# Performance work log

Measured on AMD Instinct MI355X. Metric: run time of the kernel, lower is better.

Reference implementation:

```python
import jax, jax.numpy as jnp
import numpy as np

LAMBDA_SOFTMAX = 9.0
LAMBDA_LSE = 6.0
EPS = 1e-8
LEAKY_SLOPE = 0.1


def setup_inputs() -> dict:
    key = jax.random.key(0)
    k1, k2, k3, k4 = jax.random.split(key, 4)
    B, R, L, D = 256, 36, 40, 1024  # n_image=n_caption=B, n_regions, max_words, embed
    return {
        'pool_img': jax.random.normal(k1, (B, D), jnp.float32),
        'img_emb': jax.random.normal(k2, (B, R, D), jnp.float32),
        'pool_txt': jax.random.normal(k3, (B, D), jnp.float32),
        'cap_emb': jax.random.normal(k4, (B, L, D), jnp.float32),
    }


def _l2norm(x, axis):
    return x / (jnp.sqrt(jnp.sum(x * x, axis=axis, keepdims=True)) + EPS)


def _lse_reduce(m):
    # mul_(lambda_lse).exp_() ; sum over singleton dim ; log / lambda_lse
    return jnp.log(jnp.exp(m * LAMBDA_LSE)) / LAMBDA_LSE


def _text_score_one(cap_i, txt_poo_i, images):
    # cap_i: (L, d) query; images: (B, R, d) context. clipped_l2norm variant.
    attn = jnp.einsum('brd,ld->brl', images, cap_i)            # (B, R, L)
    attn = jax.nn.leaky_relu(attn, LEAKY_SLOPE)
    attn = _l2norm(attn, axis=2)                               # l2norm over queryL
    attn = jnp.swapaxes(attn, 1, 2)                            # (B, L, R)
    attn = jax.nn.softmax(attn * LAMBDA_SOFTMAX, axis=-1)      # softmax over regions
    wctx = jnp.einsum('blr,brd->bld', attn, images)            # (B, L, d)
    w12 = jnp.einsum('bld,d->bl', wctx, txt_poo_i)
    w1 = jnp.sqrt(jnp.sum(txt_poo_i * txt_poo_i))
    w2 = jnp.sqrt(jnp.sum(wctx * wctx, axis=2))
    sim = w12 / jnp.maximum(w1 * w2, EPS)                      # (B, L)
    return _lse_reduce(jnp.mean(sim, axis=1))                  # (B,)


def _image_score_one(cap_i, img_emb, img_poo):
    # query: img_emb (B, R, d); context: cap_i (L, d) broadcast over B.
    attn = jnp.einsum('ld,brd->blr', cap_i, img_emb)           # (B, L, R)
    attn = jax.nn.leaky_relu(attn, LEAKY_SLOPE)
    attn = _l2norm(attn, axis=2)                               # l2norm over regions
    attn = jnp.swapaxes(attn, 1, 2)                            # (B, R, L)
    attn = jax.nn.softmax(attn * LAMBDA_SOFTMAX, axis=-1)      # softmax over words
    wctx = jnp.einsum('brl,ld->brd', attn, cap_i)              # (B, R, d)
    w12 = jnp.einsum('brd,bd->br', wctx, img_poo)
    w1 = jnp.sqrt(jnp.sum(img_poo * img_poo, axis=1, keepdims=True))  # (B,1)
    w2 = jnp.sqrt(jnp.sum(wctx * wctx, axis=2))                # (B, R)
    sim = w12 / jnp.maximum(w1 * w2, EPS)
    return _lse_reduce(jnp.mean(sim, axis=1))                  # (B,)


def reference(pool_img, img_emb, pool_txt, cap_emb):
    # scores_t2i: loop over captions -> vmap; result (n_cap, n_image) -> transpose
    t2i = jax.vmap(_text_score_one, in_axes=(0, 0, None))(cap_emb, pool_txt, img_emb).T
    i2t = jax.vmap(_image_score_one, in_axes=(0, None, None))(cap_emb, img_emb, pool_img).T
    base = pool_img @ pool_txt.T
    return t2i + i2t + base
```

## Files before the change

kernel.cpp:

```cpp
#include <hip/hip_runtime.h>

typedef unsigned short u16;
typedef __attribute__((ext_vector_type(8))) short bf16x8;
typedef __attribute__((ext_vector_type(4))) float f32x4;

#define D_EMB 1024
#define NBAT  256
#define AS1 __attribute__((address_space(1)))
#define AS3 __attribute__((address_space(3)))

__device__ __forceinline__ u16 f2bf(float f){
    unsigned int u = __float_as_uint(f);
    unsigned int r = (u + 0x7fffu + ((u >> 16) & 1u)) >> 16;
    return (u16)r;
}
__device__ __forceinline__ float leaky(float x){ return x > 0.f ? x : 0.1f * x; }

__device__ __forceinline__ unsigned pack2(float a, float b){
    return (__float_as_uint(a) >> 16) | (__float_as_uint(b) & 0xffff0000u);
}
__device__ __forceinline__ float unpk_lo(unsigned p){ return __uint_as_float(p << 16); }
__device__ __forceinline__ float unpk_hi(unsigned p){ return __uint_as_float(p & 0xffff0000u); }

__global__ void pack_kernel(const float* __restrict__ pool_img, const float* __restrict__ img_emb,
                            const float* __restrict__ pool_txt, const float* __restrict__ cap_emb,
                            u16* __restrict__ imgw, u16* __restrict__ capw){
    int row = blockIdx.x;
    const float* src; u16* dst;
    if (row < NBAT * 37){
        int e = row / 37, rr = row - e * 37;
        src = (rr < 36) ? (img_emb + ((size_t)e * 36 + rr) * D_EMB) : (pool_img + (size_t)e * D_EMB);
        dst = imgw + (size_t)row * D_EMB;
    } else {
        int r2 = row - NBAT * 37;
        int e = r2 / 41, rr = r2 - e * 41;
        src = (rr < 40) ? (cap_emb + ((size_t)e * 40 + rr) * D_EMB) : (pool_txt + (size_t)e * D_EMB);
        dst = capw + (size_t)r2 * D_EMB;
    }
    int t = threadIdx.x;
    float4 v = ((const float4*)src)[t];
    unsigned long long pk = (unsigned long long)f2bf(v.x)
        | ((unsigned long long)f2bf(v.y) << 16)
        | ((unsigned long long)f2bf(v.z) << 32)
        | ((unsigned long long)f2bf(v.w) << 48);
    *(unsigned long long*)(dst + (size_t)t * 4) = pk;
}

__global__ void norm_kernel(const float* __restrict__ pool_img, const float* __restrict__ pool_txt,
                            float* __restrict__ w1i, float* __restrict__ w1t){
    __shared__ float red[256];
    int v = blockIdx.x;
    const float* src = (v < 256) ? (pool_img + (size_t)v * D_EMB)
                                 : (pool_txt + (size_t)(v - 256) * D_EMB);
    int t = threadIdx.x;
    float4 x = ((const float4*)src)[t];
    red[t] = x.x*x.x + x.y*x.y + x.z*x.z + x.w*x.w;
    __syncthreads();
    for (int off = 128; off > 0; off >>= 1){
        if (t < off) red[t] += red[t + off];
        __syncthreads();
    }
    if (t == 0){
        float n = sqrtf(red[0]);
        if (v < 256) w1i[v] = n; else w1t[v - 256] = n;
    }
}

__launch_bounds__(256, 2)
__global__ void gram_kernel(const u16* __restrict__ imgw, const u16* __restrict__ capw,
                            float* __restrict__ G, float* __restrict__ H){
    __shared__ __align__(16) char gsm[6144];
    int blk = blockIdx.x;
    int tid = threadIdx.x, lane = tid & 63;
    int wave = __builtin_amdgcn_readfirstlane(tid >> 6);
    int frow = lane & 15, q = lane >> 4;

    const u16* E; float* Gout; int R;
    if (blk < NBAT){ E = imgw + (size_t)blk * 37 * D_EMB; Gout = G + (size_t)blk * 1296; R = 36; }
    else { int b = blk - NBAT; E = capw + (size_t)b * 41 * D_EMB; Gout = H + (size_t)b * 1600; R = 40; }

    {
        uint4 z = {0u,0u,0u,0u};
        for (int off = tid * 16; off < 6144; off += 4096) *(uint4*)(gsm + off) = z;
    }

    const u16* gsrc[2]; int goff[2]; bool gval[2];
    #pragma unroll
    for (int j = 0; j < 2; ++j){
        int g = wave + j * 4;
        gval[j] = false; gsrc[j] = E; goff[j] = 0;
        if (g < 6){
            int kk = g / 3, t = g - kk * 3;
            int row = t * 16 + frow;
            gsrc[j] = E + (size_t)row * D_EMB + kk * 32 + q * 8;
            goff[j] = g * 1024;
            gval[j] = (row < R);
        }
    }

    int wm = wave >> 1, wn = wave & 1;
    int nTm = wm ? 1 : 2, nTn = wn ? 1 : 2;
    f32x4 acc[2][2];
    #pragma unroll
    for (int a = 0; a < 2; ++a)
        #pragma unroll
        for (int b = 0; b < 2; ++b) acc[a][b] = (f32x4){0.f,0.f,0.f,0.f};

    for (int c = 0; c < 16; ++c){
        __syncthreads();
        #pragma unroll
        for (int j = 0; j < 2; ++j){
            if (gval[j]){
                __builtin_amdgcn_global_load_lds(
                    (const AS1 void*)(const void*)(gsrc[j] + c * 64),
                    (AS3 void*)(void*)(gsm + goff[j] + lane * 16),
                    16, 0, 0);
            }
        }
        __syncthreads();
        #pragma unroll
        for (int kk = 0; kk < 2; ++kk){
            bf16x8 fA[2], fB[2];
            #pragma unroll
            for (int mi = 0; mi < 2; ++mi)
                if (mi < nTm) fA[mi] = *(const bf16x8*)(gsm + ((kk * 3 + (wm + mi * 2)) * 64 + lane) * 16);
            #pragma unroll
            for (int ni = 0; ni < 2; ++ni)
                if (ni < nTn) fB[ni] = *(const bf16x8*)(gsm + ((kk * 3 + (wn + ni * 2)) * 64 + lane) * 16);
            #pragma unroll
            for (int mi = 0; mi < 2; ++mi)
                if (mi < nTm)
                    #pragma unroll
                    for (int ni = 0; ni < 2; ++ni)
                        if (ni < nTn)
                            acc[mi][ni] = __builtin_amdgcn_mfma_f32_16x16x32_bf16(
                                fA[mi], fB[ni], acc[mi][ni], 0, 0, 0);
        }
    }

    #pragma unroll
    for (int mi = 0; mi < 2; ++mi){
        if (mi < nTm){
            int tm = wm + mi * 2;
            #pragma unroll
            for (int ni = 0; ni < 2; ++ni){
                if (ni < nTn){
                    int tn = wn + ni * 2;
                    int col = tn * 16 + frow;
                    if (col < R){
                        #pragma unroll
                        for (int g = 0; g < 4; ++g){
                            int row = tm * 16 + q * 4 + g;
                            if (row < R) Gout[row * R + col] = acc[mi][ni][g];
                        }
                    }
                }
            }
        }
    }
}

__launch_bounds__(256, 5)
__global__ void fused_kernel(const u16* __restrict__ imgw, const u16* __restrict__ capw,
                             const float* __restrict__ G, const float* __restrict__ H,
                             const float* __restrict__ w1i, const float* __restrict__ w1t,
                             float* __restrict__ out){
    __shared__ __align__(16) char smem[26624];
    float* Call = (float*)smem;
    float* rnb  = (float*)(smem + 25160);
    float* cnb  = (float*)(smem + 25736);

    int tid  = threadIdx.x;
    int lane = tid & 63;
    int wave = __builtin_amdgcn_readfirstlane(tid >> 6);
    int frow = lane & 15, q = lane >> 4;

    int lin = blockIdx.x;
    int xcd = lin & 7;
    int s   = lin >> 3;
    int b_t = (xcd << 4) | (s & 15);
    int i_t = s >> 4;
    int b0 = b_t * 2, i0 = i_t * 2;
    const u16* Ag = imgw + (size_t)b0 * 37 * D_EMB;
    const u16* Bg = capw + (size_t)i0 * 41 * D_EMB;

    {
        uint4 z = {0u,0u,0u,0u};
        for (int off = tid * 16; off < 22528; off += 4096) *(uint4*)(smem + off) = z;
    }

    const u16* gsrc[6]; int goff[6]; bool gval[6];
    #pragma unroll
    for (int j = 0; j < 6; ++j){
        int g = wave + j * 4;
        gval[j] = false; gsrc[j] = Ag; goff[j] = 0;
        if (g < 22){
            if (g < 10){
                int tm = g % 5, kk = g / 5;
                int row = tm * 16 + frow;
                gsrc[j] = Ag + (size_t)row * D_EMB + kk * 32 + q * 8;
                goff[j] = g * 1024;
                gval[j] = (row < 74);
            } else {
                int gb = g - 10;
                int tn = gb % 6, kk = gb / 6;
                int row = tn * 16 + frow;
                gsrc[j] = Bg + (size_t)row * D_EMB + kk * 32 + q * 8;
                goff[j] = 10240 + gb * 1024;
                gval[j] = (row < 82);
            }
        }
    }

    int wm = wave >> 1, wn = wave & 1;
    int nTm = wm ? 2 : 3;
    f32x4 acc[3][3];
    #pragma unroll
    for (int aa = 0; aa < 3; ++aa)
        #pragma unroll
        for (int bb = 0; bb < 3; ++bb) acc[aa][bb] = (f32x4){0.f, 0.f, 0.f, 0.f};

    for (int c = 0; c < 16; ++c){
        __syncthreads();
        #pragma unroll
        for (int j = 0; j < 6; ++j){
            if (gval[j]){
                __builtin_amdgcn_global_load_lds(
                    (const AS1 void*)(const void*)(gsrc[j] + c * 64),
                    (AS3 void*)(void*)(smem + goff[j] + lane * 16),
                    16, 0, 0);
            }
        }
        __syncthreads();
        #pragma unroll
        for (int kk = 0; kk < 2; ++kk){
            bf16x8 bfr[3];
            #pragma unroll
            for (int ni = 0; ni < 3; ++ni){
                int tn = wn + ni * 2;
                bfr[ni] = *(const bf16x8*)(smem + 10240 + ((kk * 6 + tn) * 64 + lane) * 16);
            }
            #pragma unroll
            for (int mi = 0; mi < 3; ++mi){
                if (mi < nTm){
                    int tm = wm + mi * 2;
                    bf16x8 af = *(const bf16x8*)(smem + ((kk * 5 + tm) * 64 + lane) * 16);
                    #pragma unroll
                    for (int ni = 0; ni < 3; ++ni){
                        acc[mi][ni] = __builtin_amdgcn_mfma_f32_16x16x32_bf16(
                            af, bfr[ni], acc[mi][ni], 0, 0, 0);
                    }
                }
            }
        }
    }
    __syncthreads();

    #pragma unroll
    for (int mi = 0; mi < 3; ++mi){
        if (mi < nTm){
            int tm = wm + mi * 2;
            #pragma unroll
            for (int ni = 0; ni < 3; ++ni){
                int tn = wn + ni * 2;
                int col = tn * 16 + frow;
                int rbase = tm * 16 + q * 4;
                if (col < 82){
                    #pragma unroll
                    for (int g = 0; g < 4; ++g){
                        int rowc = rbase + g;
                        if (rowc < 74) Call[rowc * 85 + col] = acc[mi][ni][g];
                    }
                }
            }
        }
    }
    __syncthreads();

    int pb = wave >> 1, pi = wave & 1;
    int bg = b0 + pb, ig = i0 + pi;
    const float* Sv = Call + (pb * 37) * 85 + pi * 41;
    const float* Gb = G + (size_t)bg * 1296;
    const float* Hi = H + (size_t)ig * 1600;

    {
        int r0 = (lane < 36) ? lane : 35;
        float s2 = 0.f;
        #pragma unroll
        for (int l = 0; l < 40; ++l){ float x = leaky(Sv[r0 * 85 + l]); s2 = fmaf(x, x, s2); }
        if (lane < 36) rnb[wave * 36 + lane] = 1.f / (sqrtf(s2) + 1e-8f);
    }
    float t2i_sum;
    {
        int lc = (lane < 40) ? lane : 39;
        unsigned up[18];
        float dd = 0.f, num = 0.f;
        #pragma unroll
        for (int r = 0; r < 36; r += 2){
            float x0 = leaky(Sv[r * 85 + lc]);
            float e0 = __expf(9.0f * x0 * rnb[wave * 36 + r]);
            float x1 = leaky(Sv[(r + 1) * 85 + lc]);
            float e1 = __expf(9.0f * x1 * rnb[wave * 36 + r + 1]);
            dd += e0 + e1;
            num = fmaf(e0, Sv[r * 85 + 40], fmaf(e1, Sv[(r + 1) * 85 + 40], num));
            up[r >> 1] = pack2(e0, e1);
        }
        float zz = 0.f;
        #pragma unroll
        for (int rr = 0; rr < 36; ++rr){
            float urr = (rr & 1) ? unpk_hi(up[rr >> 1]) : unpk_lo(up[rr >> 1]);
            float t = 0.f;
            #pragma unroll
            for (int r2 = rr + 1; r2 < 36; ++r2){
                float ur2 = (r2 & 1) ? unpk_hi(up[r2 >> 1]) : unpk_lo(up[r2 >> 1]);
                t = fmaf(Gb[rr * 36 + r2], ur2, t);
            }
            zz += (2.f * t + Gb[rr * 36 + rr] * urr) * urr;
        }
        float w2s = sqrtf(fmaxf(zz, 0.f));
        float sim = num / fmaxf(w1t[ig] * w2s, 1e-8f);
        sim = (lane < 40) ? sim : 0.f;
        #pragma unroll
        for (int off = 32; off > 0; off >>= 1) sim += __shfl_down(sim, off);
        t2i_sum = sim;
    }

    {
        int l0 = (lane < 40) ? lane : 39;
        float s2 = 0.f;
        #pragma unroll
        for (int r = 0; r < 36; ++r){ float x = leaky(Sv[r * 85 + l0]); s2 = fmaf(x, x, s2); }
        if (lane < 40) cnb[wave * 40 + lane] = 1.f / (sqrtf(s2) + 1e-8f);
    }
    float i2t_sum;
    {
        int rc = (lane < 36) ? lane : 35;
        unsigned vp[20];
        float dd = 0.f, num = 0.f;
        #pragma unroll
        for (int l = 0; l < 40; l += 2){
            float x0 = leaky(Sv[rc * 85 + l]);
            float e0 = __expf(9.0f * x0 * cnb[wave * 40 + l]);
            float x1 = leaky(Sv[rc * 85 + l + 1]);
            float e1 = __expf(9.0f * x1 * cnb[wave * 40 + l + 1]);
            dd += e0 + e1;
            num = fmaf(e0, Sv[36 * 85 + l], fmaf(e1, Sv[36 * 85 + l + 1], num));
            vp[l >> 1] = pack2(e0, e1);
        }
        float zz = 0.f;
        #pragma unroll
        for (int ll = 0; ll < 40; ++ll){
            float vll = (ll & 1) ? unpk_hi(vp[ll >> 1]) : unpk_lo(vp[ll >> 1]);
            float t = 0.f;
            #pragma unroll
            for (int l2 = ll + 1; l2 < 40; ++l2){
                float vl2 = (l2 & 1) ? unpk_hi(vp[l2 >> 1]) : unpk_lo(vp[l2 >> 1]);
                t = fmaf(Hi[ll * 40 + l2], vl2, t);
            }
            zz += (2.f * t + Hi[ll * 40 + ll] * vll) * vll;
        }
        float w2s = sqrtf(fmaxf(zz, 0.f));
        float sim = num / fmaxf(w1i[bg] * w2s, 1e-8f);
        sim = (lane < 36) ? sim : 0.f;
        #pragma unroll
        for (int off = 32; off > 0; off >>= 1) sim += __shfl_down(sim, off);
        i2t_sum = sim;
    }

    if (lane == 0)
        out[bg * 256 + ig] = t2i_sum * (1.f / 40.f) + i2t_sum * (1.f / 36.f) + Sv[36 * 85 + 40];
}

extern "C" void kernel_launch(void* const* d_in, const int* in_sizes, int n_in,
                              void* d_out, int out_size, void* d_ws, size_t ws_size,
                              hipStream_t stream){
    const float* pool_img = (const float*)d_in[0];
    const float* img_emb  = (const float*)d_in[1];
    const float* pool_txt = (const float*)d_in[2];
    const float* cap_emb  = (const float*)d_in[3];
    float* out = (float*)d_out;

    char* ws = (char*)d_ws;
    size_t o = 0;
    u16* imgw = (u16*)(ws + o);  o += (size_t)256 * 37 * 1024 * 2;
    u16* capw = (u16*)(ws + o);  o += (size_t)256 * 41 * 1024 * 2;
    float* G  = (float*)(ws + o); o += (size_t)256 * 36 * 36 * 4;
    float* H  = (float*)(ws + o); o += (size_t)256 * 40 * 40 * 4;
    float* w1i = (float*)(ws + o); o += 1024;
    float* w1t = (float*)(ws + o); o += 1024;

    pack_kernel<<<19968, 256, 0, stream>>>(pool_img, img_emb, pool_txt, cap_emb, imgw, capw);
    norm_kernel<<<512, 256, 0, stream>>>(pool_img, pool_txt, w1i, w1t);
    gram_kernel<<<512, 256, 0, stream>>>(imgw, capw, G, H);
    fused_kernel<<<16384, 256, 0, stream>>>(imgw, capw, G, H, w1i, w1t, out);
}
```

Before: 750.6 us.

## Replace per-pair Gram quadratic forms with Cholesky factors and MFMA norms

Adds a kernel that Cholesky-factorizes each per-image and per-caption Gram matrix and stores the factors in bf16. The fused kernel then computes each weighted-context norm as ||u^T L||^2 using bf16 MFMA instructions on attention weights staged in swizzled shared memory, replacing the scalar triangular quadratic-form loops. The aim is to move the dominant O(R^2) per-lane FMA work onto matrix cores. It adds a small extra launch, lowers the occupancy hint from 5 to 4, and adds bf16 rounding of the factors and of the exp weights in the MFMA path.

```diff
diff --git a/kernel.cpp b/kernel.cpp
--- a/kernel.cpp
+++ b/kernel.cpp
@@ -19,8 +19,6 @@
 __device__ __forceinline__ unsigned pack2(float a, float b){
     return (__float_as_uint(a) >> 16) | (__float_as_uint(b) & 0xffff0000u);
 }
-__device__ __forceinline__ float unpk_lo(unsigned p){ return __uint_as_float(p << 16); }
-__device__ __forceinline__ float unpk_hi(unsigned p){ return __uint_as_float(p & 0xffff0000u); }
 
 __global__ void pack_kernel(const float* __restrict__ pool_img, const float* __restrict__ img_emb,
                             const float* __restrict__ pool_txt, const float* __restrict__ cap_emb,
@@ -160,9 +158,44 @@
     }
 }
 
-__launch_bounds__(256, 5)
+template<int R>
+__device__ __forceinline__ void chol_wave(const float* __restrict__ src,
+                                          u16* __restrict__ dst, int lane){
+    int r = lane;
+    bool act = (r < R);
+    const float* row = src + (size_t)(act ? r : 0) * R;
+    float a[R];
+    #pragma unroll
+    for (int k = 0; k < R; ++k) a[k] = act ? row[k] : 0.f;
+    #pragma unroll
+    for (int j = 0; j < R; ++j){
+        float ajj = __shfl(a[j], j);
+        float inv = (ajj > 1e-12f) ? rsqrtf(ajj) : 0.f;
+        float lrj = a[j] * inv;
+        if (r < j || !act) lrj = 0.f;
+        dst[j * 64 + lane] = f2bf(lrj);
+        #pragma unroll
+        for (int k = j + 1; k < R; ++k){
+            float lkj = __shfl(lrj, k);
+            a[k] = fmaf(-lrj, lkj, a[k]);
+        }
+    }
+    #pragma unroll
+    for (int j = R; j < 48; ++j) dst[j * 64 + lane] = 0;
+}
+
+__global__ void chol_kernel(const float* __restrict__ G, const float* __restrict__ H,
+                            u16* __restrict__ Lbi, u16* __restrict__ Lbc){
+    int lane = threadIdx.x & 63;
+    int wave = threadIdx.x >> 6;
+    int id = blockIdx.x * 4 + wave;
+    if (id < NBAT) chol_wave<36>(G + (size_t)id * 1296, Lbi + (size_t)id * 3072, lane);
+    else           chol_wave<40>(H + (size_t)(id - NBAT) * 1600, Lbc + (size_t)(id - NBAT) * 3072, lane);
+}
+
+__launch_bounds__(256, 4)
 __global__ void fused_kernel(const u16* __restrict__ imgw, const u16* __restrict__ capw,
-                             const float* __restrict__ G, const float* __restrict__ H,
+                             const u16* __restrict__ Lbi, const u16* __restrict__ Lbc,
                              const float* __restrict__ w1i, const float* __restrict__ w1t,
                              float* __restrict__ out){
     __shared__ __align__(16) char smem[26624];
@@ -280,8 +313,8 @@
     int pb = wave >> 1, pi = wave & 1;
     int bg = b0 + pb, ig = i0 + pi;
     const float* Sv = Call + (pb * 37) * 85 + pi * 41;
-    const float* Gb = G + (size_t)bg * 1296;
-    const float* Hi = H + (size_t)ig * 1600;
+    const u16* Lb_t2i = Lbi + (size_t)bg * 3072;
+    const u16* Lb_i2t = Lbc + (size_t)ig * 3072;
 
     {
         int r0 = (lane < 36) ? lane : 35;
@@ -290,41 +323,6 @@
         for (int l = 0; l < 40; ++l){ float x = leaky(Sv[r0 * 85 + l]); s2 = fmaf(x, x, s2); }
         if (lane < 36) rnb[wave * 36 + lane] = 1.f / (sqrtf(s2) + 1e-8f);
     }
-    float t2i_sum;
-    {
-        int lc = (lane < 40) ? lane : 39;
-        unsigned up[18];
-        float dd = 0.f, num = 0.f;
-        #pragma unroll
-        for (int r = 0; r < 36; r += 2){
-            float x0 = leaky(Sv[r * 85 + lc]);
-            float e0 = __expf(9.0f * x0 * rnb[wave * 36 + r]);
-            float x1 = leaky(Sv[(r + 1) * 85 + lc]);
-            float e1 = __expf(9.0f * x1 * rnb[wave * 36 + r + 1]);
-            dd += e0 + e1;
-            num = fmaf(e0, Sv[r * 85 + 40], fmaf(e1, Sv[(r + 1) * 85 + 40], num));
-            up[r >> 1] = pack2(e0, e1);
-        }
-        float zz = 0.f;
-        #pragma unroll
-        for (int rr = 0; rr < 36; ++rr){
-            float urr = (rr & 1) ? unpk_hi(up[rr >> 1]) : unpk_lo(up[rr >> 1]);
-            float t = 0.f;
-            #pragma unroll
-            for (int r2 = rr + 1; r2 < 36; ++r2){
-                float ur2 = (r2 & 1) ? unpk_hi(up[r2 >> 1]) : unpk_lo(up[r2 >> 1]);
-                t = fmaf(Gb[rr * 36 + r2], ur2, t);
-            }
-            zz += (2.f * t + Gb[rr * 36 + rr] * urr) * urr;
-        }
-        float w2s = sqrtf(fmaxf(zz, 0.f));
-        float sim = num / fmaxf(w1t[ig] * w2s, 1e-8f);
-        sim = (lane < 40) ? sim : 0.f;
-        #pragma unroll
-        for (int off = 32; off > 0; off >>= 1) sim += __shfl_down(sim, off);
-        t2i_sum = sim;
-    }
-
     {
         int l0 = (lane < 40) ? lane : 39;
         float s2 = 0.f;
@@ -332,43 +330,161 @@
         for (int r = 0; r < 36; ++r){ float x = leaky(Sv[r * 85 + l0]); s2 = fmaf(x, x, s2); }
         if (lane < 40) cnb[wave * 40 + lane] = 1.f / (sqrtf(s2) + 1e-8f);
     }
-    float i2t_sum;
+
+    unsigned up[18]; float num1 = 0.f;
+    {
+        int lc = (lane < 40) ? lane : 39;
+        #pragma unroll
+        for (int r = 0; r < 36; r += 2){
+            float x0 = leaky(Sv[r * 85 + lc]) * rnb[wave * 36 + r];
+            float x1 = leaky(Sv[(r + 1) * 85 + lc]) * rnb[wave * 36 + r + 1];
+            float e0 = __expf(9.0f * x0), e1 = __expf(9.0f * x1);
+            num1 = fmaf(e0, Sv[r * 85 + 40], fmaf(e1, Sv[(r + 1) * 85 + 40], num1));
+            up[r >> 1] = pack2(e0, e1);
+        }
+    }
+    unsigned vp[20]; float num2 = 0.f;
     {
         int rc = (lane < 36) ? lane : 35;
-        unsigned vp[20];
-        float dd = 0.f, num = 0.f;
         #pragma unroll
         for (int l = 0; l < 40; l += 2){
-            float x0 = leaky(Sv[rc * 85 + l]);
-            float e0 = __expf(9.0f * x0 * cnb[wave * 40 + l]);
-            float x1 = leaky(Sv[rc * 85 + l + 1]);
-            float e1 = __expf(9.0f * x1 * cnb[wave * 40 + l + 1]);
-            dd += e0 + e1;
-            num = fmaf(e0, Sv[36 * 85 + l], fmaf(e1, Sv[36 * 85 + l + 1], num));
+            float x0 = leaky(Sv[rc * 85 + l]) * cnb[wave * 40 + l];
+            float x1 = leaky(Sv[rc * 85 + l + 1]) * cnb[wave * 40 + l + 1];
+            float e0 = __expf(9.0f * x0), e1 = __expf(9.0f * x1);
+            num2 = fmaf(e0, Sv[36 * 85 + l], fmaf(e1, Sv[36 * 85 + l + 1], num2));
             vp[l >> 1] = pack2(e0, e1);
         }
-        float zz = 0.f;
-        #pragma unroll
-        for (int ll = 0; ll < 40; ++ll){
-            float vll = (ll & 1) ? unpk_hi(vp[ll >> 1]) : unpk_lo(vp[ll >> 1]);
-            float t = 0.f;
-            #pragma unroll
-            for (int l2 = ll + 1; l2 < 40; ++l2){
-                float vl2 = (l2 & 1) ? unpk_hi(vp[l2 >> 1]) : unpk_lo(vp[l2 >> 1]);
-                t = fmaf(Hi[ll * 40 + l2], vl2, t);
-            }
-            zz += (2.f * t + Hi[ll * 40 + ll] * vll) * vll;
-        }
-        float w2s = sqrtf(fmaxf(zz, 0.f));
-        float sim = num / fmaxf(w1i[bg] * w2s, 1e-8f);
-        sim = (lane < 36) ? sim : 0.f;
-        #pragma unroll
-        for (int off = 32; off > 0; off >>= 1) sim += __shfl_down(sim, off);
-        i2t_sum = sim;
+    }
+    float base = Sv[36 * 85 + 40];
+    __syncthreads();
+
+    char* slice = smem + wave * 6144;
+    int sxw = lane & 7;
+
+    if (lane < 40){
+        char* rp = slice + lane * 128;
+        #pragma unroll
+        for (int jj = 0; jj < 9; ++jj){
+            int slot = jj >> 1, wi = (jj & 1) * 8;
+            uint2 w; w.x = up[jj * 2]; w.y = up[jj * 2 + 1];
+            *(uint2*)(rp + ((slot ^ sxw) * 16 + wi)) = w;
+        }
+        uint2 z2; z2.x = 0u; z2.y = 0u;
+        *(uint2*)(rp + ((4 ^ sxw) * 16 + 8)) = z2;
+        uint4 z4 = {0u,0u,0u,0u};
+        #pragma unroll
+        for (int slot = 5; slot < 8; ++slot)
+            *(uint4*)(rp + ((slot ^ sxw) * 16)) = z4;
+    }
+
+    float tsum;
+    {
+        f32x4 pacc[3][3];
+        #pragma unroll
+        for (int aa = 0; aa < 3; ++aa)
+            #pragma unroll
+            for (int bb = 0; bb < 3; ++bb) pacc[aa][bb] = (f32x4){0.f,0.f,0.f,0.f};
+        #pragma unroll
+        for (int kk = 0; kk < 2; ++kk){
+            bf16x8 afr[3];
+            #pragma unroll
+            for (int mt = 0; mt < 3; ++mt){
+                int row = mt * 16 + frow;
+                afr[mt] = *(const bf16x8*)(slice + row * 128 + (((kk * 4 + q) ^ (row & 7)) * 16));
+            }
+            #pragma unroll
+            for (int nt = 0; nt < 3; ++nt){
+                bf16x8 bfr = *(const bf16x8*)(Lb_t2i + (nt * 16 + frow) * 64 + kk * 32 + q * 8);
+                #pragma unroll
+                for (int mt = 0; mt < 3; ++mt)
+                    pacc[mt][nt] = __builtin_amdgcn_mfma_f32_16x16x32_bf16(
+                        afr[mt], bfr, pacc[mt][nt], 0, 0, 0);
+            }
+        }
+        float w1 = w1t[ig];
+        tsum = 0.f;
+        #pragma unroll
+        for (int mt = 0; mt < 3; ++mt){
+            #pragma unroll
+            for (int g = 0; g < 4; ++g){
+                float sv = pacc[mt][0][g] * pacc[mt][0][g]
+                         + pacc[mt][1][g] * pacc[mt][1][g];
+                float t2 = pacc[mt][2][g] * pacc[mt][2][g];
+                sv += (frow < 4) ? t2 : 0.f;
+                sv += __shfl_xor(sv, 1); sv += __shfl_xor(sv, 2);
+                sv += __shfl_xor(sv, 4); sv += __shfl_xor(sv, 8);
+                int m = mt * 16 + 4 * q + g;
+                float nm = __shfl(num1, m);
+                float sim = nm / fmaxf(w1 * sqrtf(sv), 1e-8f);
+                tsum += (m < 40) ? sim : 0.f;
+            }
+        }
+        tsum += __shfl_xor(tsum, 16);
+        tsum += __shfl_xor(tsum, 32);
+    }
+
+    if (lane < 36){
+        char* rp = slice + lane * 128;
+        #pragma unroll
+        for (int jj = 0; jj < 10; ++jj){
+            int slot = jj >> 1, wi = (jj & 1) * 8;
+            uint2 w; w.x = vp[jj * 2]; w.y = vp[jj * 2 + 1];
+            *(uint2*)(rp + ((slot ^ sxw) * 16 + wi)) = w;
+        }
+        uint4 z4 = {0u,0u,0u,0u};
+        #pragma unroll
+        for (int slot = 5; slot < 8; ++slot)
+            *(uint4*)(rp + ((slot ^ sxw) * 16)) = z4;
+    }
+
+    float isum;
+    {
+        f32x4 pacc[3][3];
+        #pragma unroll
+        for (int aa = 0; aa < 3; ++aa)
+            #pragma unroll
+            for (int bb = 0; bb < 3; ++bb) pacc[aa][bb] = (f32x4){0.f,0.f,0.f,0.f};
+        #pragma unroll
+        for (int kk = 0; kk < 2; ++kk){
+            bf16x8 afr[3];
+            #pragma unroll
+            for (int mt = 0; mt < 3; ++mt){
+                int row = mt * 16 + frow;
+                afr[mt] = *(const bf16x8*)(slice + row * 128 + (((kk * 4 + q) ^ (row & 7)) * 16));
+            }
+            #pragma unroll
+            for (int nt = 0; nt < 3; ++nt){
+                bf16x8 bfr = *(const bf16x8*)(Lb_i2t + (nt * 16 + frow) * 64 + kk * 32 + q * 8);
+                #pragma unroll
+                for (int mt = 0; mt < 3; ++mt)
+                    pacc[mt][nt] = __builtin_amdgcn_mfma_f32_16x16x32_bf16(
+                        afr[mt], bfr, pacc[mt][nt], 0, 0, 0);
+            }
+        }
+        float w1 = w1i[bg];
+        isum = 0.f;
+        #pragma unroll
+        for (int mt = 0; mt < 3; ++mt){
+            #pragma unroll
+            for (int g = 0; g < 4; ++g){
+                float sv = pacc[mt][0][g] * pacc[mt][0][g]
+                         + pacc[mt][1][g] * pacc[mt][1][g];
+                float t2 = pacc[mt][2][g] * pacc[mt][2][g];
+                sv += (frow < 8) ? t2 : 0.f;
+                sv += __shfl_xor(sv, 1); sv += __shfl_xor(sv, 2);
+                sv += __shfl_xor(sv, 4); sv += __shfl_xor(sv, 8);
+                int m = mt * 16 + 4 * q + g;
+                float nm = __shfl(num2, m);
+                float sim = nm / fmaxf(w1 * sqrtf(sv), 1e-8f);
+                isum += (m < 36) ? sim : 0.f;
+            }
+        }
+        isum += __shfl_xor(isum, 16);
+        isum += __shfl_xor(isum, 32);
     }
 
     if (lane == 0)
-        out[bg * 256 + ig] = t2i_sum * (1.f / 40.f) + i2t_sum * (1.f / 36.f) + Sv[36 * 85 + 40];
+        out[bg * 256 + ig] = tsum * (1.f / 40.f) + isum * (1.f / 36.f) + base;
 }
 
 extern "C" void kernel_launch(void* const* d_in, const int* in_sizes, int n_in,
@@ -388,9 +504,12 @@
     float* H  = (float*)(ws + o); o += (size_t)256 * 40 * 40 * 4;
     float* w1i = (float*)(ws + o); o += 1024;
     float* w1t = (float*)(ws + o); o += 1024;
+    u16* Lbi = (u16*)(ws + o); o += (size_t)256 * 48 * 64 * 2;
+    u16* Lbc = (u16*)(ws + o); o += (size_t)256 * 48 * 64 * 2;
 
     pack_kernel<<<19968, 256, 0, stream>>>(pool_img, img_emb, pool_txt, cap_emb, imgw, capw);
     norm_kernel<<<512, 256, 0, stream>>>(pool_img, pool_txt, w1i, w1t);
     gram_kernel<<<512, 256, 0, stream>>>(imgw, capw, G, H);
-    fused_kernel<<<16384, 256, 0, stream>>>(imgw, capw, G, H, w1i, w1t, out);
-}
+    chol_kernel<<<128, 256, 0, stream>>>(G, H, Lbi, Lbc);
+    fused_kernel<<<16384, 256, 0, stream>>>(imgw, capw, Lbi, Lbc, w1i, w1t, out);
+}
```

Result: slower. 829.3 us (+10.5%).

## Use packed fp16 dot2 for Gram quadratic forms and fold norm into pack kernel

Applied to the files above, without the earlier changes.

Converts the precomputed Gram matrices G and H to packed fp16 in a new small kernel. The softmax weights are also kept as packed fp16, so the per-wave quadratic form u^T G u uses fdot2 over the full matrix instead of scalar fp32 FMAs over the upper triangle. It also folds the softmax scale of 9 into the inverse norms and merges the pooled-vector norm computation into pack_kernel, removing one launch. This cuts ALU work and global load bytes in the hot fused kernel, at the cost of fp16 rounding of G, H and the exp weights (overflow risk for large Gram entries) and one extra small launch.

```diff
diff --git a/kernel.cpp b/kernel.cpp
--- a/kernel.cpp
+++ b/kernel.cpp
@@ -3,6 +3,7 @@
 typedef unsigned short u16;
 typedef __attribute__((ext_vector_type(8))) short bf16x8;
 typedef __attribute__((ext_vector_type(4))) float f32x4;
+typedef __attribute__((ext_vector_type(2))) __fp16 h16x2;
 
 #define D_EMB 1024
 #define NBAT  256
@@ -16,26 +17,35 @@
 }
 __device__ __forceinline__ float leaky(float x){ return x > 0.f ? x : 0.1f * x; }
 
-__device__ __forceinline__ unsigned pack2(float a, float b){
-    return (__float_as_uint(a) >> 16) | (__float_as_uint(b) & 0xffff0000u);
-}
-__device__ __forceinline__ float unpk_lo(unsigned p){ return __uint_as_float(p << 16); }
-__device__ __forceinline__ float unpk_hi(unsigned p){ return __uint_as_float(p & 0xffff0000u); }
+__device__ __forceinline__ float dot2h(h16x2 a, h16x2 b, float c){
+#if __has_builtin(__builtin_amdgcn_fdot2)
+    return __builtin_amdgcn_fdot2(a, b, c, false);
+#else
+    return fmaf((float)a[0], (float)b[0], fmaf((float)a[1], (float)b[1], c));
+#endif
+}
 
 __global__ void pack_kernel(const float* __restrict__ pool_img, const float* __restrict__ img_emb,
                             const float* __restrict__ pool_txt, const float* __restrict__ cap_emb,
-                            u16* __restrict__ imgw, u16* __restrict__ capw){
+                            u16* __restrict__ imgw, u16* __restrict__ capw,
+                            float* __restrict__ w1i, float* __restrict__ w1t){
+    __shared__ float red[256];
     int row = blockIdx.x;
     const float* src; u16* dst;
+    bool is_pool; float* wout;
     if (row < NBAT * 37){
         int e = row / 37, rr = row - e * 37;
+        is_pool = (rr == 36);
         src = (rr < 36) ? (img_emb + ((size_t)e * 36 + rr) * D_EMB) : (pool_img + (size_t)e * D_EMB);
         dst = imgw + (size_t)row * D_EMB;
+        wout = w1i + e;
     } else {
         int r2 = row - NBAT * 37;
         int e = r2 / 41, rr = r2 - e * 41;
+        is_pool = (rr == 40);
         src = (rr < 40) ? (cap_emb + ((size_t)e * 40 + rr) * D_EMB) : (pool_txt + (size_t)e * D_EMB);
         dst = capw + (size_t)r2 * D_EMB;
+        wout = w1t + e;
     }
     int t = threadIdx.x;
     float4 v = ((const float4*)src)[t];
@@ -44,25 +54,14 @@
         | ((unsigned long long)f2bf(v.z) << 32)
         | ((unsigned long long)f2bf(v.w) << 48);
     *(unsigned long long*)(dst + (size_t)t * 4) = pk;
-}
-
-__global__ void norm_kernel(const float* __restrict__ pool_img, const float* __restrict__ pool_txt,
-                            float* __restrict__ w1i, float* __restrict__ w1t){
-    __shared__ float red[256];
-    int v = blockIdx.x;
-    const float* src = (v < 256) ? (pool_img + (size_t)v * D_EMB)
-                                 : (pool_txt + (size_t)(v - 256) * D_EMB);
-    int t = threadIdx.x;
-    float4 x = ((const float4*)src)[t];
-    red[t] = x.x*x.x + x.y*x.y + x.z*x.z + x.w*x.w;
-    __syncthreads();
-    for (int off = 128; off > 0; off >>= 1){
-        if (t < off) red[t] += red[t + off];
+    if (is_pool){
+        red[t] = v.x*v.x + v.y*v.y + v.z*v.z + v.w*v.w;
         __syncthreads();
-    }
-    if (t == 0){
-        float n = sqrtf(red[0]);
-        if (v < 256) w1i[v] = n; else w1t[v - 256] = n;
+        for (int off = 128; off > 0; off >>= 1){
+            if (t < off) red[t] += red[t + off];
+            __syncthreads();
+        }
+        if (t == 0) *wout = sqrtf(red[0]);
     }
 }
 
@@ -160,9 +159,26 @@
     }
 }
 
+__global__ void ghpack_kernel(const float* __restrict__ G, const float* __restrict__ H,
+                              h16x2* __restrict__ Gh, h16x2* __restrict__ Hh){
+    int id = blockIdx.x;
+    int t = threadIdx.x;
+    if (id < NBAT){
+        const float* src = G + (size_t)id * 1296;
+        h16x2* dst = Gh + (size_t)id * 648;
+        for (int i = t; i < 648; i += 256)
+            dst[i] = __builtin_amdgcn_cvt_pkrtz(src[2 * i], src[2 * i + 1]);
+    } else {
+        const float* src = H + (size_t)(id - NBAT) * 1600;
+        h16x2* dst = Hh + (size_t)(id - NBAT) * 800;
+        for (int i = t; i < 800; i += 256)
+            dst[i] = __builtin_amdgcn_cvt_pkrtz(src[2 * i], src[2 * i + 1]);
+    }
+}
+
 __launch_bounds__(256, 5)
 __global__ void fused_kernel(const u16* __restrict__ imgw, const u16* __restrict__ capw,
-                             const float* __restrict__ G, const float* __restrict__ H,
+                             const h16x2* __restrict__ Gh, const h16x2* __restrict__ Hh,
                              const float* __restrict__ w1i, const float* __restrict__ w1t,
                              float* __restrict__ out){
     __shared__ __align__(16) char smem[26624];
@@ -280,42 +296,36 @@
     int pb = wave >> 1, pi = wave & 1;
     int bg = b0 + pb, ig = i0 + pi;
     const float* Sv = Call + (pb * 37) * 85 + pi * 41;
-    const float* Gb = G + (size_t)bg * 1296;
-    const float* Hi = H + (size_t)ig * 1600;
+    const h16x2* Gp = Gh + (size_t)bg * 648;
+    const h16x2* Hp = Hh + (size_t)ig * 800;
 
     {
         int r0 = (lane < 36) ? lane : 35;
         float s2 = 0.f;
         #pragma unroll
         for (int l = 0; l < 40; ++l){ float x = leaky(Sv[r0 * 85 + l]); s2 = fmaf(x, x, s2); }
-        if (lane < 36) rnb[wave * 36 + lane] = 1.f / (sqrtf(s2) + 1e-8f);
+        if (lane < 36) rnb[wave * 36 + lane] = 9.f / (sqrtf(s2) + 1e-8f);
     }
     float t2i_sum;
     {
         int lc = (lane < 40) ? lane : 39;
-        unsigned up[18];
-        float dd = 0.f, num = 0.f;
+        h16x2 uh[18];
+        float num = 0.f;
         #pragma unroll
         for (int r = 0; r < 36; r += 2){
-            float x0 = leaky(Sv[r * 85 + lc]);
-            float e0 = __expf(9.0f * x0 * rnb[wave * 36 + r]);
-            float x1 = leaky(Sv[(r + 1) * 85 + lc]);
-            float e1 = __expf(9.0f * x1 * rnb[wave * 36 + r + 1]);
-            dd += e0 + e1;
+            float e0 = __expf(leaky(Sv[r * 85 + lc] * rnb[wave * 36 + r]));
+            float e1 = __expf(leaky(Sv[(r + 1) * 85 + lc] * rnb[wave * 36 + r + 1]));
             num = fmaf(e0, Sv[r * 85 + 40], fmaf(e1, Sv[(r + 1) * 85 + 40], num));
-            up[r >> 1] = pack2(e0, e1);
+            uh[r >> 1] = __builtin_amdgcn_cvt_pkrtz(e0, e1);
         }
         float zz = 0.f;
         #pragma unroll
         for (int rr = 0; rr < 36; ++rr){
-            float urr = (rr & 1) ? unpk_hi(up[rr >> 1]) : unpk_lo(up[rr >> 1]);
-            float t = 0.f;
-            #pragma unroll
-            for (int r2 = rr + 1; r2 < 36; ++r2){
-                float ur2 = (r2 & 1) ? unpk_hi(up[r2 >> 1]) : unpk_lo(up[r2 >> 1]);
-                t = fmaf(Gb[rr * 36 + r2], ur2, t);
-            }
-            zz += (2.f * t + Gb[rr * 36 + rr] * urr) * urr;
+            float w = 0.f;
+            #pragma unroll
+            for (int j = 0; j < 18; ++j)
+                w = dot2h(uh[j], Gp[rr * 18 + j], w);
+            zz = fmaf((float)uh[rr >> 1][rr & 1], w, zz);
         }
         float w2s = sqrtf(fmaxf(zz, 0.f));
         float sim = num / fmaxf(w1t[ig] * w2s, 1e-8f);
@@ -330,34 +340,28 @@
         float s2 = 0.f;
         #pragma unroll
         for (int r = 0; r < 36; ++r){ float x = leaky(Sv[r * 85 + l0]); s2 = fmaf(x, x, s2); }
-        if (lane < 40) cnb[wave * 40 + lane] = 1.f / (sqrtf(s2) + 1e-8f);
+        if (lane < 40) cnb[wave * 40 + lane] = 9.f / (sqrtf(s2) + 1e-8f);
     }
     float i2t_sum;
     {
         int rc = (lane < 36) ? lane : 35;
-        unsigned vp[20];
-        float dd = 0.f, num = 0.f;
+        h16x2 vh[20];
+        float num = 0.f;
         #pragma unroll
         for (int l = 0; l < 40; l += 2){
-            float x0 = leaky(Sv[rc * 85 + l]);
-            float e0 = __expf(9.0f * x0 * cnb[wave * 40 + l]);
-            float x1 = leaky(Sv[rc * 85 + l + 1]);
-            float e1 = __expf(9.0f * x1 * cnb[wave * 40 + l + 1]);
-            dd += e0 + e1;
+            float e0 = __expf(leaky(Sv[rc * 85 + l] * cnb[wave * 40 + l]));
+            float e1 = __expf(leaky(Sv[rc * 85 + l + 1] * cnb[wave * 40 + l + 1]));
             num = fmaf(e0, Sv[36 * 85 + l], fmaf(e1, Sv[36 * 85 + l + 1], num));
-            vp[l >> 1] = pack2(e0, e1);
+            vh[l >> 1] = __builtin_amdgcn_cvt_pkrtz(e0, e1);
         }
         float zz = 0.f;
         #pragma unroll
         for (int ll = 0; ll < 40; ++ll){
-            float vll = (ll & 1) ? unpk_hi(vp[ll >> 1]) : unpk_lo(vp[ll >> 1]);
-            float t = 0.f;
-            #pragma unroll
-            for (int l2 = ll + 1; l2 < 40; ++l2){
-                float vl2 = (l2 & 1) ? unpk_hi(vp[l2 >> 1]) : unpk_lo(vp[l2 >> 1]);
-                t = fmaf(Hi[ll * 40 + l2], vl2, t);
-            }
-            zz += (2.f * t + Hi[ll * 40 + ll] * vll) * vll;
+            float w = 0.f;
+            #pragma unroll
+            for (int j = 0; j < 20; ++j)
+                w = dot2h(vh[j], Hp[ll * 20 + j], w);
+            zz = fmaf((float)vh[ll >> 1][ll & 1], w, zz);
         }
         float w2s = sqrtf(fmaxf(zz, 0.f));
         float sim = num / fmaxf(w1i[bg] * w2s, 1e-8f);
@@ -388,9 +392,12 @@
     float* H  = (float*)(ws + o); o += (size_t)256 * 40 * 40 * 4;
     float* w1i = (float*)(ws + o); o += 1024;
     float* w1t = (float*)(ws + o); o += 1024;
-
-    pack_kernel<<<19968, 256, 0, stream>>>(pool_img, img_emb, pool_txt, cap_emb, imgw, capw);
-    norm_kernel<<<512, 256, 0, stream>>>(pool_img, pool_txt, w1i, w1t);
+    h16x2* Gh = (h16x2*)(ws + o); o += (size_t)256 * 648 * 4;
+    h16x2* Hh = (h16x2*)(ws + o); o += (size_t)256 * 800 * 4;
+
+    pack_kernel<<<19968, 256, 0, stream>>>(pool_img, img_emb, pool_txt, cap_emb,
+                                           imgw, capw, w1i, w1t);
     gram_kernel<<<512, 256, 0, stream>>>(imgw, capw, G, H);
-    fused_kernel<<<16384, 256, 0, stream>>>(imgw, capw, G, H, w1i, w1t, out);
-}
+    ghpack_kernel<<<512, 256, 0, stream>>>(G, H, Gh, Hh);
+    fused_kernel<<<16384, 256, 0, stream>>>(imgw, capw, Gh, Hh, w1i, w1t, out);
+}
```

Result: faster. 722.1 us (-3.8%).
